# Kernel optimization log

Hardware: AMD Instinct MI355X
Metric: run time of the kernel (lower is better)

## Reference

```python
import jax, jax.numpy as jnp
import numpy as np

B, N, E, F, H, OUT = 128, 2048, 16384, 32, 64, 16


def setup_inputs() -> dict:
    key = jax.random.key(0)
    ks = jax.random.split(key, 8)
    node_features = jax.random.normal(ks[0], (B, N, F), jnp.float32)
    edge_index = jax.random.randint(ks[1], (B, 2, E), 0, N)
    n_nodes = jax.random.randint(ks[2], (B,), N // 2, N + 1)
    # prefix node mask (required for the original's index-consistency)
    node_mask = jnp.arange(N)[None, :] < n_nodes[:, None]
    glorot = lambda k, sh, fan: jax.random.normal(k, sh, jnp.float32) / np.sqrt(fan)
    return dict(
        node_features=node_features, edge_index=edge_index, node_mask=node_mask,
        W1=glorot(ks[3], (F, H), F), b1=jnp.zeros((H,), jnp.float32),
        W2=glorot(ks[4], (H, H), H), b2=jnp.zeros((H,), jnp.float32),
        aW1=glorot(ks[5], (H, H), H), ab1=jnp.zeros((H,), jnp.float32),
        aW2=glorot(ks[6], (H, OUT), H), ab2=jnp.zeros((OUT,), jnp.float32),
    )


def reference(node_features, edge_index, node_mask, W1, b1, W2, b2, aW1, ab1, aW2, ab2):
    x = node_features
    src, dst = edge_index[:, 0], edge_index[:, 1]          # [B,E] source->target
    n = node_mask.sum(-1)                                   # [B] valid nodes per graph
    max_idx = n - 1
    emask = (src <= max_idx[:, None]) & (dst <= max_idx[:, None])
    w = emask.astype(x.dtype)                               # [B,E] edge weights

    # flatten batch into one big segment space [B*N]
    offs = (jnp.arange(B, dtype=src.dtype) * N)[:, None]
    src_f = (src + offs).reshape(-1)
    dst_f = (dst + offs).reshape(-1)
    w_f = w.reshape(-1)

    # GCN normalization with self-loops (PyG GCNConv default)
    deg = jax.ops.segment_sum(w_f, dst_f, num_segments=B * N).reshape(B, N)
    deg = deg + node_mask.astype(x.dtype)                   # self-loop weight 1 on valid nodes
    dis = jnp.where(deg > 0, jax.lax.rsqrt(deg), 0.0)       # deg^{-1/2}, [B,N]
    dis_f = dis.reshape(-1)
    norm = dis_f[src_f] * dis_f[dst_f] * w_f                # [B*E]
    nmask_f = node_mask.reshape(-1).astype(x.dtype)[:, None]
    nmask = node_mask.astype(x.dtype)[..., None]

    def gcn_relu(h, W, bias):
        hW = (h @ W).reshape(B * N, -1)                     # transform first (PyG order)
        msgs = hW[src_f] * norm[:, None]                    # [B*E, H]
        agg = jax.ops.segment_sum(msgs, dst_f, num_segments=B * N)
        agg = agg + hW * ((dis * dis).reshape(-1)[:, None] * nmask_f)  # self-loop term
        out = (agg.reshape(B, N, -1) + bias) * nmask
        return jax.nn.relu(out)

    h1 = gcn_relu(x * nmask, W1, b1)
    h2 = gcn_relu(h1, W2, b2)

    # mean pool over valid nodes (zeros if empty graph)
    pooled = h2.sum(1) / jnp.maximum(n, 1)[:, None].astype(x.dtype)
    hidden = jax.nn.relu(pooled @ aW1 + ab1)
    logits = hidden @ aW2 + ab2                             # [B, OUT]
    return logits
```

## Files before the change

kernel.cpp:

```cpp
#include <hip/hip_runtime.h>
#include <hip/hip_bf16.h>

#define B 128
#define N 2048
#define E 16384
#define F 32
#define H 64
#define OUTD 16
#define CAP 16
#define NP1 (N + 1)

typedef __attribute__((ext_vector_type(8))) short bf16x8;
typedef __attribute__((ext_vector_type(4))) float f32x4;

__device__ __forceinline__ float b2f(unsigned short u) {
    return __uint_as_float(((unsigned int)u) << 16);
}
__device__ __forceinline__ unsigned short f2b(float f) {
    unsigned int x = __float_as_uint(f);
    unsigned int r = (x + 0x7FFFu + ((x >> 16) & 1u)) >> 16;
    return (unsigned short)r;
}
__device__ __forceinline__ unsigned int pack2(float a, float b) {
    return (unsigned int)f2b(a) | ((unsigned int)f2b(b) << 16);
}

__device__ __forceinline__ void unpack8(float (&a)[8], uint4 u) {
    a[0] += __uint_as_float(u.x << 16);
    a[1] += __uint_as_float(u.x & 0xffff0000u);
    a[2] += __uint_as_float(u.y << 16);
    a[3] += __uint_as_float(u.y & 0xffff0000u);
    a[4] += __uint_as_float(u.z << 16);
    a[5] += __uint_as_float(u.z & 0xffff0000u);
    a[6] += __uint_as_float(u.w << 16);
    a[7] += __uint_as_float(u.w & 0xffff0000u);
}

struct PrepArgs {
    const void* src[9];
    void* dst[9];
};

__global__ __launch_bounds__(256) void k_prep(PrepArgs pa, int* flags) {
    const int bid = blockIdx.x;
    const int t = threadIdx.x;
    int sz;
    switch (bid) {
        case 0: sz = B * N * F; break;
        case 1: sz = F * H; break;
        case 2: sz = H; break;
        case 3: sz = H * H; break;
        case 4: sz = H; break;
        case 5: sz = H * H; break;
        case 6: sz = H; break;
        case 7: sz = H * OUTD; break;
        default: sz = OUTD; break;
    }
    const int K = sz < 1024 ? sz : 1024;
    const unsigned short* p = (const unsigned short*)pa.src[bid];
    float s = 0.f;
    for (int i = t; i < K; i += 256) s += fminf(fabsf(b2f(p[i])), 1e6f);
    __shared__ float red[256];
    __shared__ int isbf;
    red[t] = s;
    __syncthreads();
    for (int st = 128; st > 0; st >>= 1) {
        if (t < st) red[t] += red[t + st];
        __syncthreads();
    }
    if (t == 0) {
        int f = (red[0] < 100.0f * (float)K) ? 1 : 0;
        isbf = f;
        if (bid == 0) flags[0] = f;
    }
    __syncthreads();
    if (bid == 0) return;
    const int fl = isbf;
    auto rd = [&](int i) -> float {
        return fl ? b2f(((const unsigned short*)pa.src[bid])[i])
                  : ((const float*)pa.src[bid])[i];
    };
    if (bid == 1) {
        unsigned short* dst = (unsigned short*)pa.dst[bid];
        for (int i = t; i < F * H; i += 256) {
            int k = i >> 6, n2 = i & 63;
            dst[n2 * 40 + k] = f2b(rd(i));
        }
    } else if (bid == 3) {
        unsigned short* dst = (unsigned short*)pa.dst[bid];
        for (int i = t; i < H * H; i += 256) {
            int k = i >> 6, n2 = i & 63;
            dst[n2 * 72 + k] = f2b(rd(i));
        }
    } else {
        float* dst = (float*)pa.dst[bid];
        for (int i = t; i < sz; i += 256) dst[i] = rd(i);
    }
}

__global__ __launch_bounds__(1024) void k_build(
    const int* __restrict__ eidx, const void* __restrict__ mask,
    int* __restrict__ n_arr, float* __restrict__ dis,
    unsigned char* __restrict__ degc, unsigned short* __restrict__ ssrc,
    int2* __restrict__ ovf, int* __restrict__ ovf_cnt,
    float* __restrict__ pooled, unsigned int* __restrict__ y_u,
    unsigned int* __restrict__ z_u) {
    __shared__ int s_cnt[N];
    __shared__ int s_w[16];
    __shared__ int s_n;
    __shared__ int s_ovf;
    const int b = blockIdx.x;
    const int t = threadIdx.x;
    const int bN = b * N;
    const unsigned char* mb = (const unsigned char*)mask;
    int mode;
    if (mb[0] == 0x80 && mb[1] == 0x3F) mode = 2;
    else if (mb[0] != 0 && mb[1] != 0) mode = 0;
    else if (mb[0] != 0) mode = (mb[4] != 0) ? 1 : 4;
    else mode = 3;
    int cnt = 0;
    if (mode == 0) {
        const unsigned char* r = mb + (size_t)b * N;
        for (int i = t; i < N; i += 1024) cnt += (r[i] != 0);
    } else if (mode == 1 || mode == 3) {
        const unsigned int* r = (const unsigned int*)mask + (size_t)b * N;
        for (int i = t; i < N; i += 1024) cnt += (r[i] != 0);
    } else if (mode == 2) {
        const unsigned short* r = (const unsigned short*)mask + (size_t)b * N;
        for (int i = t; i < N; i += 1024) cnt += (r[i] != 0);
    } else {
        const unsigned long long* r = (const unsigned long long*)mask + (size_t)b * N;
        for (int i = t; i < N; i += 1024) cnt += (r[i] != 0ULL);
    }
    for (int o = 32; o > 0; o >>= 1) cnt += __shfl_down(cnt, o);
    if ((t & 63) == 0) s_w[t >> 6] = cnt;
    for (int i = t; i < N; i += 1024) s_cnt[i] = 0;
    if (t == 0) s_ovf = 0;
    __syncthreads();
    if (t == 0) {
        int a = 0;
        for (int i = 0; i < 16; i++) a += s_w[i];
        s_n = a > N ? N : a;
    }
    __syncthreads();
    const int n = s_n;
    const int4* es4 = (const int4*)(eidx + (size_t)b * 2 * E);
    const int4* ed4 = es4 + E / 4;
    for (int i = t; i < E / 4; i += 1024) {
        int4 s4 = es4[i], d4 = ed4[i];
        if ((unsigned)s4.x < (unsigned)n && (unsigned)d4.x < (unsigned)n) atomicAdd(&s_cnt[d4.x], 1);
        if ((unsigned)s4.y < (unsigned)n && (unsigned)d4.y < (unsigned)n) atomicAdd(&s_cnt[d4.y], 1);
        if ((unsigned)s4.z < (unsigned)n && (unsigned)d4.z < (unsigned)n) atomicAdd(&s_cnt[d4.z], 1);
        if ((unsigned)s4.w < (unsigned)n && (unsigned)d4.w < (unsigned)n) atomicAdd(&s_cnt[d4.w], 1);
    }
    {
        const int4 iv = make_int4(0x08000800, 0x08000800, 0x08000800, 0x08000800);
        int4* sp4 = (int4*)(ssrc + (size_t)bN * CAP);
        for (int i = t; i < N * CAP / 8; i += 1024) sp4[i] = iv;
    }
    if (t < 16) y_u[((size_t)b * NP1 + N) * (F / 2) + t] = 0u;
    if (t >= 32 && t < 64) z_u[((size_t)b * NP1 + N) * (H / 2) + (t - 32)] = 0u;
    __syncthreads();
    for (int v = t; v < N; v += 1024) {
        int c = s_cnt[v];
        dis[bN + v] = (v < n) ? rsqrtf((float)(c + 1)) : 0.0f;
        degc[bN + v] = (unsigned char)(c < CAP ? c : CAP);
        s_cnt[v] = 0;
    }
    __syncthreads();
    for (int i = t; i < E / 4; i += 1024) {
        int4 s4 = es4[i], d4 = ed4[i];
#define FILL1(SS, DD)                                                          \
        if ((unsigned)(SS) < (unsigned)n && (unsigned)(DD) < (unsigned)n) {    \
            int pos = atomicAdd(&s_cnt[DD], 1);                                \
            if (pos < CAP)                                                     \
                ssrc[((size_t)(bN + (DD))) * CAP + pos] = (unsigned short)(SS);\
            else {                                                             \
                int oi = atomicAdd(&s_ovf, 1);                                 \
                if (oi < E) ovf[(size_t)b * E + oi] = make_int2((DD), (SS));   \
            }                                                                  \
        }
        FILL1(s4.x, d4.x) FILL1(s4.y, d4.y) FILL1(s4.z, d4.z) FILL1(s4.w, d4.w)
#undef FILL1
    }
    if (t == 0) { n_arr[b] = n; ovf_cnt[b] = s_ovf; }
    if (t < H) pooled[b * H + t] = 0.0f;
}

__global__ __launch_bounds__(256) void k_premult(
    const void* __restrict__ x, const int* __restrict__ bf16flag,
    const float* __restrict__ dis, unsigned int* __restrict__ y_u) {
    const int gid = blockIdx.x * 256 + threadIdx.x;
    const int g = gid >> 4;
    const int f2 = gid & 15;
    const int b = g >> 11;
    const int v = g & (N - 1);
    const float dv = dis[g];
    float a, c;
    if (*bf16flag) {
        const unsigned short* xp = (const unsigned short*)x + (size_t)g * F + 2 * f2;
        a = b2f(xp[0]); c = b2f(xp[1]);
    } else {
        const float* xp = (const float*)x + (size_t)g * F + 2 * f2;
        a = xp[0]; c = xp[1];
    }
    y_u[((size_t)b * NP1 + v) * (F / 2) + f2] = pack2(a * dv, c * dv);
}

__global__ __launch_bounds__(256) void k_agg_gemm1(
    const unsigned int* __restrict__ y_u, const float* __restrict__ dis,
    const unsigned char* __restrict__ degc, const unsigned short* __restrict__ ssrc,
    const int2* __restrict__ ovf, const int* __restrict__ ovf_cnt,
    const unsigned short* __restrict__ w1t, const float* __restrict__ b1f,
    unsigned short* __restrict__ zs) {
    __shared__ unsigned short s_e[64 * CAP];
    __shared__ unsigned char s_dg[64];
    __shared__ float s_dv[64];
    __shared__ float s_b1[64];
    __shared__ __align__(16) unsigned short s_w1t[64 * 40];
    __shared__ __align__(16) unsigned short s_a1[64 * 40];
    const int bid = blockIdx.x;
    const int b = (bid & 7) + ((bid >> 8) << 3);
    const int v0 = ((bid >> 3) & 31) * 64;
    const int t = threadIdx.x;
    const int bN = b * N;
    if (t < 128) ((int4*)s_e)[t] = ((const int4*)(ssrc + (size_t)(bN + v0) * CAP))[t];
    if (t >= 128 && t < 144)
        ((unsigned int*)s_dg)[t - 128] = ((const unsigned int*)(degc + bN + v0))[t - 128];
    if (t >= 192) s_dv[t - 192] = dis[bN + v0 + (t - 192)];
    if (t >= 144 && t < 208) s_b1[t - 144] = b1f[t - 144];
    for (int i = t; i < 320; i += 256) ((int4*)s_w1t)[i] = ((const int4*)w1t)[i];
    __syncthreads();
    const int lane = t & 63;
    const int w = t >> 6;
    const int oc = ovf_cnt[b];
    const unsigned int* yb = y_u + (size_t)b * NP1 * (F / 2);
    {
        const int nn = w * 16 + (lane >> 2);
        const int v = v0 + nn;
        const int cu = (lane & 3) * 4;
        int md = s_dg[w * 16 + (lane & 15)];
        int m2;
        m2 = __shfl_xor(md, 1); md = md > m2 ? md : m2;
        m2 = __shfl_xor(md, 2); md = md > m2 ? md : m2;
        m2 = __shfl_xor(md, 4); md = md > m2 ? md : m2;
        m2 = __shfl_xor(md, 8); md = md > m2 ? md : m2;
        const unsigned short* ep = &s_e[nn * CAP];
        float a[8] = {0.f, 0.f, 0.f, 0.f, 0.f, 0.f, 0.f, 0.f};
        uint4 cur = *(const uint4*)(yb + (size_t)v * (F / 2) + cu);
        uint4 nxt = *(const uint4*)(yb + (size_t)ep[0] * (F / 2) + cu);
        for (int s = 0; s < md; s++) {
            int sn = s + 1; sn = sn > CAP - 1 ? CAP - 1 : sn;
            uint4 n2 = *(const uint4*)(yb + (size_t)ep[sn] * (F / 2) + cu);
            unpack8(a, cur);
            cur = nxt; nxt = n2;
        }
        unpack8(a, cur);
        if (oc > 0) {
            const int2* ob = ovf + (size_t)b * E;
            for (int j = 0; j < oc; j++) {
                int2 o = ob[j];
                if (o.x == v) {
                    uint4 u4 = *(const uint4*)(yb + (size_t)o.y * (F / 2) + cu);
                    unpack8(a, u4);
                }
            }
        }
        const float dv = s_dv[nn];
        uint4 ov;
        ov.x = pack2(a[0] * dv, a[1] * dv);
        ov.y = pack2(a[2] * dv, a[3] * dv);
        ov.z = pack2(a[4] * dv, a[5] * dv);
        ov.w = pack2(a[6] * dv, a[7] * dv);
        *(uint4*)((unsigned int*)s_a1 + nn * 20 + cu) = ov;
    }
    __syncthreads();
    const int quad = lane >> 4;
    const int f2 = lane & 15;
    const int m0 = w * 16;
    bf16x8 af = *(const bf16x8*)&s_a1[(m0 + f2) * 40 + quad * 8];
    float dvr[4];
#pragma unroll
    for (int r = 0; r < 4; r++) dvr[r] = s_dv[m0 + quad * 4 + r];
#pragma unroll
    for (int nt = 0; nt < 4; nt++) {
        bf16x8 bf = *(const bf16x8*)&s_w1t[(nt * 16 + f2) * 40 + quad * 8];
        f32x4 acc = {0.f, 0.f, 0.f, 0.f};
        acc = __builtin_amdgcn_mfma_f32_16x16x32_bf16(af, bf, acc, 0, 0, 0);
        float bb = s_b1[nt * 16 + f2];
#pragma unroll
        for (int r = 0; r < 4; r++) {
            int row = m0 + quad * 4 + r;
            float val = dvr[r] * fmaxf(acc[r] + bb, 0.0f);
            zs[((size_t)b * NP1 + v0 + row) * H + nt * 16 + f2] = f2b(val);
        }
    }
}

__global__ __launch_bounds__(256) void k_agg_gemm2_pool(
    const unsigned int* __restrict__ z_u, const float* __restrict__ dis,
    const unsigned char* __restrict__ degc, const unsigned short* __restrict__ ssrc,
    const int2* __restrict__ ovf, const int* __restrict__ ovf_cnt,
    const unsigned short* __restrict__ w2t, const float* __restrict__ b2f_,
    float* __restrict__ pooled) {
    __shared__ unsigned short s_e[64 * CAP];
    __shared__ unsigned char s_dg[64];
    __shared__ float s_dv[64];
    __shared__ float s_b2[64];
    __shared__ __align__(16) unsigned short s_w2t[64 * 72];
    __shared__ __align__(16) unsigned short s_a2[64 * 72];
    __shared__ float s_pool[4][64];
    const int bid = blockIdx.x;
    const int b = (bid & 7) + ((bid >> 8) << 3);
    const int v0 = ((bid >> 3) & 31) * 64;
    const int t = threadIdx.x;
    const int bN = b * N;
    if (t < 128) ((int4*)s_e)[t] = ((const int4*)(ssrc + (size_t)(bN + v0) * CAP))[t];
    if (t >= 128 && t < 144)
        ((unsigned int*)s_dg)[t - 128] = ((const unsigned int*)(degc + bN + v0))[t - 128];
    if (t >= 192) s_dv[t - 192] = dis[bN + v0 + (t - 192)];
    if (t >= 144 && t < 208) s_b2[t - 144] = b2f_[t - 144];
    for (int i = t; i < 576; i += 256) ((int4*)s_w2t)[i] = ((const int4*)w2t)[i];
    __syncthreads();
    const int lane = t & 63;
    const int w = t >> 6;
    const int oc = ovf_cnt[b];
    const unsigned int* zb = z_u + (size_t)b * NP1 * (H / 2);
#pragma unroll
    for (int g = 0; g < 2; g++) {
        const int nn = w * 16 + g * 8 + (lane >> 3);
        const int v = v0 + nn;
        const int cu = (lane & 7) * 4;
        int md = s_dg[w * 16 + g * 8 + (lane & 7)];
        int m2;
        m2 = __shfl_xor(md, 1); md = md > m2 ? md : m2;
        m2 = __shfl_xor(md, 2); md = md > m2 ? md : m2;
        m2 = __shfl_xor(md, 4); md = md > m2 ? md : m2;
        const unsigned short* ep = &s_e[nn * CAP];
        float a[8] = {0.f, 0.f, 0.f, 0.f, 0.f, 0.f, 0.f, 0.f};
        uint4 cur = *(const uint4*)(zb + (size_t)v * (H / 2) + cu);
        uint4 nxt = *(const uint4*)(zb + (size_t)ep[0] * (H / 2) + cu);
        for (int s = 0; s < md; s++) {
            int sn = s + 1; sn = sn > CAP - 1 ? CAP - 1 : sn;
            uint4 n2 = *(const uint4*)(zb + (size_t)ep[sn] * (H / 2) + cu);
            unpack8(a, cur);
            cur = nxt; nxt = n2;
        }
        unpack8(a, cur);
        if (oc > 0) {
            const int2* ob = ovf + (size_t)b * E;
            for (int j = 0; j < oc; j++) {
                int2 o = ob[j];
                if (o.x == v) {
                    uint4 u4 = *(const uint4*)(zb + (size_t)o.y * (H / 2) + cu);
                    unpack8(a, u4);
                }
            }
        }
        const float dv = s_dv[nn];
        uint4 ov;
        ov.x = pack2(a[0] * dv, a[1] * dv);
        ov.y = pack2(a[2] * dv, a[3] * dv);
        ov.z = pack2(a[4] * dv, a[5] * dv);
        ov.w = pack2(a[6] * dv, a[7] * dv);
        *(uint4*)((unsigned int*)s_a2 + nn * 36 + cu) = ov;
    }
    __syncthreads();
    const int quad = lane >> 4;
    const int f2 = lane & 15;
    const int m0 = w * 16;
    bf16x8 af0 = *(const bf16x8*)&s_a2[(m0 + f2) * 72 + quad * 8];
    bf16x8 af1 = *(const bf16x8*)&s_a2[(m0 + f2) * 72 + 32 + quad * 8];
    float dvr[4];
#pragma unroll
    for (int r = 0; r < 4; r++) dvr[r] = s_dv[m0 + quad * 4 + r];
#pragma unroll
    for (int nt = 0; nt < 4; nt++) {
        bf16x8 bf0 = *(const bf16x8*)&s_w2t[(nt * 16 + f2) * 72 + quad * 8];
        bf16x8 bf1 = *(const bf16x8*)&s_w2t[(nt * 16 + f2) * 72 + 32 + quad * 8];
        f32x4 acc = {0.f, 0.f, 0.f, 0.f};
        acc = __builtin_amdgcn_mfma_f32_16x16x32_bf16(af0, bf0, acc, 0, 0, 0);
        acc = __builtin_amdgcn_mfma_f32_16x16x32_bf16(af1, bf1, acc, 0, 0, 0);
        float bb = s_b2[nt * 16 + f2];
        float ps = 0.f;
#pragma unroll
        for (int r = 0; r < 4; r++)
            ps += (dvr[r] > 0.0f) ? fmaxf(acc[r] + bb, 0.0f) : 0.0f;
        ps += __shfl_xor(ps, 16);
        ps += __shfl_xor(ps, 32);
        if (quad == 0) s_pool[w][nt * 16 + f2] = ps;
    }
    __syncthreads();
    if (t < H)
        atomicAdd(&pooled[b * H + t],
                  s_pool[0][t] + s_pool[1][t] + s_pool[2][t] + s_pool[3][t]);
}

__global__ __launch_bounds__(64) void k_mlp(
    const float* __restrict__ pooled, const int* __restrict__ n_arr,
    const float* __restrict__ aW1, const float* __restrict__ ab1,
    const float* __restrict__ aW2, const float* __restrict__ ab2,
    const int* __restrict__ flags, void* __restrict__ out) {
    const int b = blockIdx.x;
    const int t = threadIdx.x;
    __shared__ float p[64];
    __shared__ float hid[64];
    int n = n_arr[b];
    if (n < 1) n = 1;
    p[t] = pooled[b * H + t] / (float)n;
    __syncthreads();
    float acc = ab1[t];
    for (int j = 0; j < 64; j++) acc += p[j] * aW1[j * 64 + t];
    hid[t] = fmaxf(acc, 0.0f);
    __syncthreads();
    if (t < 16) {
        float a2 = ab2[t];
        for (int j = 0; j < 64; j++) a2 += hid[j] * aW2[j * 16 + t];
        if (flags[0]) ((unsigned short*)out)[b * OUTD + t] = f2b(a2);
        else          ((float*)out)[b * OUTD + t] = a2;
    }
}

extern "C" void kernel_launch(void* const* d_in, const int* in_sizes, int n_in,
                              void* d_out, int out_size, void* d_ws, size_t ws_size,
                              hipStream_t stream) {
    const void* x    = d_in[0];
    const int*  eidx = (const int*)d_in[1];
    const void* mask = d_in[2];

    char* ws = (char*)d_ws;
    size_t off = 0;
    auto alloc = [&](size_t bytes) -> void* {
        void* p = ws + off;
        off += (bytes + 255) & ~(size_t)255;
        return p;
    };
    int*   flags   = (int*)alloc(16 * sizeof(int));
    unsigned short* w1t = (unsigned short*)alloc(64 * 40 * 2);
    unsigned short* w2t = (unsigned short*)alloc(64 * 72 * 2);
    float* b1f     = (float*)alloc(H * sizeof(float));
    float* b2f_    = (float*)alloc(H * sizeof(float));
    float* aW1f    = (float*)alloc(H * H * sizeof(float));
    float* ab1f    = (float*)alloc(H * sizeof(float));
    float* aW2f    = (float*)alloc(H * OUTD * sizeof(float));
    float* ab2f    = (float*)alloc(OUTD * sizeof(float));
    int*   n_arr   = (int*)alloc(B * sizeof(int));
    float* dis     = (float*)alloc((size_t)B * N * sizeof(float));
    unsigned char*  degc = (unsigned char*)alloc((size_t)B * N);
    unsigned short* ssrc = (unsigned short*)alloc((size_t)B * N * CAP * 2);
    int2*  ovf     = (int2*)alloc((size_t)B * E * sizeof(int2));
    int*   ovf_cnt = (int*)alloc(B * sizeof(int));
    float* pooled  = (float*)alloc((size_t)B * H * sizeof(float));
    unsigned int* y_u = (unsigned int*)alloc((size_t)B * NP1 * (F / 2) * 4);
    unsigned int* z_u = (unsigned int*)alloc((size_t)B * NP1 * (H / 2) * 4);

    PrepArgs pa;
    pa.src[0] = x;        pa.dst[0] = pooled;
    pa.src[1] = d_in[3];  pa.dst[1] = w1t;
    pa.src[2] = d_in[4];  pa.dst[2] = b1f;
    pa.src[3] = d_in[5];  pa.dst[3] = w2t;
    pa.src[4] = d_in[6];  pa.dst[4] = b2f_;
    pa.src[5] = d_in[7];  pa.dst[5] = aW1f;
    pa.src[6] = d_in[8];  pa.dst[6] = ab1f;
    pa.src[7] = d_in[9];  pa.dst[7] = aW2f;
    pa.src[8] = d_in[10]; pa.dst[8] = ab2f;

    k_prep<<<9, 256, 0, stream>>>(pa, flags);
    k_build<<<B, 1024, 0, stream>>>(eidx, mask, n_arr, dis, degc, ssrc, ovf,
                                    ovf_cnt, pooled, y_u, z_u);
    k_premult<<<(B * N * (F / 2)) / 256, 256, 0, stream>>>(x, flags, dis, y_u);
    k_agg_gemm1<<<B * 32, 256, 0, stream>>>(y_u, dis, degc, ssrc, ovf, ovf_cnt,
                                            w1t, b1f, (unsigned short*)z_u);
    k_agg_gemm2_pool<<<B * 32, 256, 0, stream>>>(z_u, dis, degc, ssrc, ovf,
                                                 ovf_cnt, w2t, b2f_, pooled);
    k_mlp<<<B, 64, 0, stream>>>(pooled, n_arr, aW1f, ab1f, aW2f, ab2f, flags, d_out);
}
```

Baseline: 173.9 us.

## Fuse prep, premult and MLP into neighbouring kernels; single-pass CSR build

The weight-prep and dtype-detection kernel is merged into k_build. The separate degree-count pass over edges is dropped: slots are filled in one atomic pass and degrees are read from the final counters. The premultiply kernel is removed, so gemm1 gathers raw features and scales each neighbour by its own dis value. The MLP head runs in the last block of each graph, found with a done counter and threadfence, and the sentinel padding rows and their initialisation are removed by masking indices. This cuts three launches and one full pass over node features, in exchange for extra per-edge dis loads and a serialized tail block per graph.

```diff
diff --git a/kernel.cpp b/kernel.cpp
--- a/kernel.cpp
+++ b/kernel.cpp
@@ -8,7 +8,6 @@
 #define H 64
 #define OUTD 16
 #define CAP 16
-#define NP1 (N + 1)
 
 typedef __attribute__((ext_vector_type(8))) short bf16x8;
 typedef __attribute__((ext_vector_type(4))) float f32x4;
@@ -25,7 +24,17 @@
     return (unsigned int)f2b(a) | ((unsigned int)f2b(b) << 16);
 }
 
-__device__ __forceinline__ void unpack8(float (&a)[8], uint4 u) {
+__device__ __forceinline__ void fma8(float (&a)[8], uint4 u, float w) {
+    a[0] = fmaf(__uint_as_float(u.x << 16), w, a[0]);
+    a[1] = fmaf(__uint_as_float(u.x & 0xffff0000u), w, a[1]);
+    a[2] = fmaf(__uint_as_float(u.y << 16), w, a[2]);
+    a[3] = fmaf(__uint_as_float(u.y & 0xffff0000u), w, a[3]);
+    a[4] = fmaf(__uint_as_float(u.z << 16), w, a[4]);
+    a[5] = fmaf(__uint_as_float(u.z & 0xffff0000u), w, a[5]);
+    a[6] = fmaf(__uint_as_float(u.w << 16), w, a[6]);
+    a[7] = fmaf(__uint_as_float(u.w & 0xffff0000u), w, a[7]);
+}
+__device__ __forceinline__ void add8(float (&a)[8], uint4 u) {
     a[0] += __uint_as_float(u.x << 16);
     a[1] += __uint_as_float(u.x & 0xffff0000u);
     a[2] += __uint_as_float(u.y << 16);
@@ -41,77 +50,35 @@
     void* dst[9];
 };
 
-__global__ __launch_bounds__(256) void k_prep(PrepArgs pa, int* flags) {
-    const int bid = blockIdx.x;
-    const int t = threadIdx.x;
-    int sz;
-    switch (bid) {
-        case 0: sz = B * N * F; break;
-        case 1: sz = F * H; break;
-        case 2: sz = H; break;
-        case 3: sz = H * H; break;
-        case 4: sz = H; break;
-        case 5: sz = H * H; break;
-        case 6: sz = H; break;
-        case 7: sz = H * OUTD; break;
-        default: sz = OUTD; break;
-    }
-    const int K = sz < 1024 ? sz : 1024;
-    const unsigned short* p = (const unsigned short*)pa.src[bid];
-    float s = 0.f;
-    for (int i = t; i < K; i += 256) s += fminf(fabsf(b2f(p[i])), 1e6f);
-    __shared__ float red[256];
-    __shared__ int isbf;
-    red[t] = s;
-    __syncthreads();
-    for (int st = 128; st > 0; st >>= 1) {
-        if (t < st) red[t] += red[t + st];
-        __syncthreads();
-    }
-    if (t == 0) {
-        int f = (red[0] < 100.0f * (float)K) ? 1 : 0;
-        isbf = f;
-        if (bid == 0) flags[0] = f;
-    }
-    __syncthreads();
-    if (bid == 0) return;
-    const int fl = isbf;
-    auto rd = [&](int i) -> float {
-        return fl ? b2f(((const unsigned short*)pa.src[bid])[i])
-                  : ((const float*)pa.src[bid])[i];
-    };
-    if (bid == 1) {
-        unsigned short* dst = (unsigned short*)pa.dst[bid];
-        for (int i = t; i < F * H; i += 256) {
-            int k = i >> 6, n2 = i & 63;
-            dst[n2 * 40 + k] = f2b(rd(i));
-        }
-    } else if (bid == 3) {
-        unsigned short* dst = (unsigned short*)pa.dst[bid];
-        for (int i = t; i < H * H; i += 256) {
-            int k = i >> 6, n2 = i & 63;
-            dst[n2 * 72 + k] = f2b(rd(i));
-        }
-    } else {
-        float* dst = (float*)pa.dst[bid];
-        for (int i = t; i < sz; i += 256) dst[i] = rd(i);
-    }
-}
-
 __global__ __launch_bounds__(1024) void k_build(
-    const int* __restrict__ eidx, const void* __restrict__ mask,
+    const void* __restrict__ x, const int* __restrict__ eidx,
+    const void* __restrict__ mask, PrepArgs pa, int* __restrict__ flags,
     int* __restrict__ n_arr, float* __restrict__ dis,
     unsigned char* __restrict__ degc, unsigned short* __restrict__ ssrc,
     int2* __restrict__ ovf, int* __restrict__ ovf_cnt,
-    float* __restrict__ pooled, unsigned int* __restrict__ y_u,
-    unsigned int* __restrict__ z_u) {
+    float* __restrict__ pooled, int* __restrict__ done,
+    unsigned int* __restrict__ y_u) {
     __shared__ int s_cnt[N];
+    __shared__ float s_fred[16];
     __shared__ int s_w[16];
-    __shared__ int s_n;
-    __shared__ int s_ovf;
+    __shared__ int s_n, s_ovf, s_xbf, s_pf;
     const int b = blockIdx.x;
     const int t = threadIdx.x;
     const int bN = b * N;
+    {
+        const unsigned short* p = (const unsigned short*)x;
+        float s = (t < 1024) ? fminf(fabsf(b2f(p[t])), 1e6f) : 0.f;
+        for (int o = 32; o > 0; o >>= 1) s += __shfl_down(s, o);
+        if ((t & 63) == 0) s_fred[t >> 6] = s;
+        __syncthreads();
+        if (t == 0) {
+            float a = 0.f;
+            for (int i = 0; i < 16; i++) a += s_fred[i];
+            int f = (a < 100.0f * 1024.0f) ? 1 : 0;
+            s_xbf = f;
+            if (b == 0) flags[0] = f;
+        }
+    }
     const unsigned char* mb = (const unsigned char*)mask;
     int mode;
     if (mb[0] == 0x80 && mb[1] == 0x3F) mode = 2;
@@ -135,39 +102,17 @@
     for (int o = 32; o > 0; o >>= 1) cnt += __shfl_down(cnt, o);
     if ((t & 63) == 0) s_w[t >> 6] = cnt;
     for (int i = t; i < N; i += 1024) s_cnt[i] = 0;
-    if (t == 0) s_ovf = 0;
     __syncthreads();
     if (t == 0) {
         int a = 0;
         for (int i = 0; i < 16; i++) a += s_w[i];
         s_n = a > N ? N : a;
+        s_ovf = 0;
     }
     __syncthreads();
     const int n = s_n;
     const int4* es4 = (const int4*)(eidx + (size_t)b * 2 * E);
     const int4* ed4 = es4 + E / 4;
-    for (int i = t; i < E / 4; i += 1024) {
-        int4 s4 = es4[i], d4 = ed4[i];
-        if ((unsigned)s4.x < (unsigned)n && (unsigned)d4.x < (unsigned)n) atomicAdd(&s_cnt[d4.x], 1);
-        if ((unsigned)s4.y < (unsigned)n && (unsigned)d4.y < (unsigned)n) atomicAdd(&s_cnt[d4.y], 1);
-        if ((unsigned)s4.z < (unsigned)n && (unsigned)d4.z < (unsigned)n) atomicAdd(&s_cnt[d4.z], 1);
-        if ((unsigned)s4.w < (unsigned)n && (unsigned)d4.w < (unsigned)n) atomicAdd(&s_cnt[d4.w], 1);
-    }
-    {
-        const int4 iv = make_int4(0x08000800, 0x08000800, 0x08000800, 0x08000800);
-        int4* sp4 = (int4*)(ssrc + (size_t)bN * CAP);
-        for (int i = t; i < N * CAP / 8; i += 1024) sp4[i] = iv;
-    }
-    if (t < 16) y_u[((size_t)b * NP1 + N) * (F / 2) + t] = 0u;
-    if (t >= 32 && t < 64) z_u[((size_t)b * NP1 + N) * (H / 2) + (t - 32)] = 0u;
-    __syncthreads();
-    for (int v = t; v < N; v += 1024) {
-        int c = s_cnt[v];
-        dis[bN + v] = (v < n) ? rsqrtf((float)(c + 1)) : 0.0f;
-        degc[bN + v] = (unsigned char)(c < CAP ? c : CAP);
-        s_cnt[v] = 0;
-    }
-    __syncthreads();
     for (int i = t; i < E / 4; i += 1024) {
         int4 s4 = es4[i], d4 = ed4[i];
 #define FILL1(SS, DD)                                                          \
@@ -183,37 +128,79 @@
         FILL1(s4.x, d4.x) FILL1(s4.y, d4.y) FILL1(s4.z, d4.z) FILL1(s4.w, d4.w)
 #undef FILL1
     }
-    if (t == 0) { n_arr[b] = n; ovf_cnt[b] = s_ovf; }
+    __syncthreads();
+    for (int v = t; v < N; v += 1024) {
+        int c = s_cnt[v];
+        dis[bN + v] = (v < n) ? rsqrtf((float)(c + 1)) : 0.0f;
+        degc[bN + v] = (unsigned char)(c < CAP ? c : CAP);
+    }
     if (t < H) pooled[b * H + t] = 0.0f;
-}
-
-__global__ __launch_bounds__(256) void k_premult(
-    const void* __restrict__ x, const int* __restrict__ bf16flag,
-    const float* __restrict__ dis, unsigned int* __restrict__ y_u) {
-    const int gid = blockIdx.x * 256 + threadIdx.x;
-    const int g = gid >> 4;
-    const int f2 = gid & 15;
-    const int b = g >> 11;
-    const int v = g & (N - 1);
-    const float dv = dis[g];
-    float a, c;
-    if (*bf16flag) {
-        const unsigned short* xp = (const unsigned short*)x + (size_t)g * F + 2 * f2;
-        a = b2f(xp[0]); c = b2f(xp[1]);
-    } else {
-        const float* xp = (const float*)x + (size_t)g * F + 2 * f2;
-        a = xp[0]; c = xp[1];
-    }
-    y_u[((size_t)b * NP1 + v) * (F / 2) + f2] = pack2(a * dv, c * dv);
+    if (t == 0) { n_arr[b] = n; ovf_cnt[b] = s_ovf; done[b] = 0; }
+    if (!s_xbf) {
+        const float4* xp = (const float4*)((const float*)x + (size_t)bN * F);
+        uint2* yp = (uint2*)(y_u + (size_t)bN * (F / 2));
+        for (int i = t; i < N * F / 4; i += 1024) {
+            float4 v = xp[i];
+            yp[i] = make_uint2(pack2(v.x, v.y), pack2(v.z, v.w));
+        }
+    }
+    if (b >= 1 && b <= 8) {
+        int sz;
+        switch (b) {
+            case 1: sz = F * H; break;
+            case 2: sz = H; break;
+            case 3: sz = H * H; break;
+            case 4: sz = H; break;
+            case 5: sz = H * H; break;
+            case 6: sz = H; break;
+            case 7: sz = H * OUTD; break;
+            default: sz = OUTD; break;
+        }
+        const int K = sz < 1024 ? sz : 1024;
+        const unsigned short* p = (const unsigned short*)pa.src[b];
+        float s = (t < K) ? fminf(fabsf(b2f(p[t])), 1e6f) : 0.f;
+        for (int o = 32; o > 0; o >>= 1) s += __shfl_down(s, o);
+        __syncthreads();
+        if ((t & 63) == 0) s_fred[t >> 6] = s;
+        __syncthreads();
+        if (t == 0) {
+            float a = 0.f;
+            for (int i = 0; i < 16; i++) a += s_fred[i];
+            s_pf = (a < 100.0f * (float)K) ? 1 : 0;
+        }
+        __syncthreads();
+        const int fl = s_pf;
+        auto rd = [&](int i) -> float {
+            return fl ? b2f(((const unsigned short*)pa.src[b])[i])
+                      : ((const float*)pa.src[b])[i];
+        };
+        if (b == 1) {
+            unsigned short* dst = (unsigned short*)pa.dst[b];
+            for (int i = t; i < F * H; i += 1024) {
+                int k = i >> 6, n2 = i & 63;
+                dst[n2 * 40 + k] = f2b(rd(i));
+            }
+        } else if (b == 3) {
+            unsigned short* dst = (unsigned short*)pa.dst[b];
+            for (int i = t; i < H * H; i += 1024) {
+                int k = i >> 6, n2 = i & 63;
+                dst[n2 * 72 + k] = f2b(rd(i));
+            }
+        } else {
+            float* dst = (float*)pa.dst[b];
+            for (int i = t; i < sz; i += 1024) dst[i] = rd(i);
+        }
+    }
 }
 
 __global__ __launch_bounds__(256) void k_agg_gemm1(
-    const unsigned int* __restrict__ y_u, const float* __restrict__ dis,
+    const void* __restrict__ x, const unsigned int* __restrict__ y_conv,
+    const int* __restrict__ flags, const float* __restrict__ dis,
     const unsigned char* __restrict__ degc, const unsigned short* __restrict__ ssrc,
     const int2* __restrict__ ovf, const int* __restrict__ ovf_cnt,
     const unsigned short* __restrict__ w1t, const float* __restrict__ b1f,
     unsigned short* __restrict__ zs) {
-    __shared__ unsigned short s_e[64 * CAP];
+    __shared__ unsigned short s_e[64 * CAP + 32];
     __shared__ unsigned char s_dg[64];
     __shared__ float s_dv[64];
     __shared__ float s_b1[64];
@@ -234,45 +221,45 @@
     const int lane = t & 63;
     const int w = t >> 6;
     const int oc = ovf_cnt[b];
-    const unsigned int* yb = y_u + (size_t)b * NP1 * (F / 2);
+    const unsigned int* yb =
+        (flags[0] ? (const unsigned int*)x : y_conv) + (size_t)bN * (F / 2);
+    const float* disb = dis + bN;
     {
         const int nn = w * 16 + (lane >> 2);
         const int v = v0 + nn;
         const int cu = (lane & 3) * 4;
-        int md = s_dg[w * 16 + (lane & 15)];
-        int m2;
-        m2 = __shfl_xor(md, 1); md = md > m2 ? md : m2;
-        m2 = __shfl_xor(md, 2); md = md > m2 ? md : m2;
-        m2 = __shfl_xor(md, 4); md = md > m2 ? md : m2;
-        m2 = __shfl_xor(md, 8); md = md > m2 ? md : m2;
+        const int dg = s_dg[nn];
+        const float dv = s_dv[nn];
         const unsigned short* ep = &s_e[nn * CAP];
         float a[8] = {0.f, 0.f, 0.f, 0.f, 0.f, 0.f, 0.f, 0.f};
-        uint4 cur = *(const uint4*)(yb + (size_t)v * (F / 2) + cu);
-        uint4 nxt = *(const uint4*)(yb + (size_t)ep[0] * (F / 2) + cu);
-        for (int s = 0; s < md; s++) {
-            int sn = s + 1; sn = sn > CAP - 1 ? CAP - 1 : sn;
-            uint4 n2 = *(const uint4*)(yb + (size_t)ep[sn] * (F / 2) + cu);
-            unpack8(a, cur);
-            cur = nxt; nxt = n2;
-        }
-        unpack8(a, cur);
+        uint4 rs = *(const uint4*)(yb + (size_t)v * (F / 2) + cu);
+        fma8(a, rs, dv);
+        for (int s = 0; s < dg; s += 2) {
+            int i0 = ep[s] & (N - 1);
+            int i1 = ep[s + 1] & (N - 1);
+            float w0 = disb[i0];
+            float w1 = (s + 1 < dg) ? disb[i1] : 0.f;
+            uint4 r0 = *(const uint4*)(yb + (size_t)i0 * (F / 2) + cu);
+            uint4 r1 = *(const uint4*)(yb + (size_t)i1 * (F / 2) + cu);
+            fma8(a, r0, w0);
+            fma8(a, r1, w1);
+        }
         if (oc > 0) {
             const int2* ob = ovf + (size_t)b * E;
             for (int j = 0; j < oc; j++) {
                 int2 o = ob[j];
                 if (o.x == v) {
                     uint4 u4 = *(const uint4*)(yb + (size_t)o.y * (F / 2) + cu);
-                    unpack8(a, u4);
+                    fma8(a, u4, disb[o.y]);
                 }
             }
         }
-        const float dv = s_dv[nn];
-        uint4 ov;
-        ov.x = pack2(a[0] * dv, a[1] * dv);
-        ov.y = pack2(a[2] * dv, a[3] * dv);
-        ov.z = pack2(a[4] * dv, a[5] * dv);
-        ov.w = pack2(a[6] * dv, a[7] * dv);
-        *(uint4*)((unsigned int*)s_a1 + nn * 20 + cu) = ov;
+        uint4 ovv;
+        ovv.x = pack2(a[0] * dv, a[1] * dv);
+        ovv.y = pack2(a[2] * dv, a[3] * dv);
+        ovv.z = pack2(a[4] * dv, a[5] * dv);
+        ovv.w = pack2(a[6] * dv, a[7] * dv);
+        *(uint4*)((unsigned int*)s_a1 + nn * 20 + cu) = ovv;
     }
     __syncthreads();
     const int quad = lane >> 4;
@@ -292,7 +279,7 @@
         for (int r = 0; r < 4; r++) {
             int row = m0 + quad * 4 + r;
             float val = dvr[r] * fmaxf(acc[r] + bb, 0.0f);
-            zs[((size_t)b * NP1 + v0 + row) * H + nt * 16 + f2] = f2b(val);
+            zs[(size_t)(bN + v0 + row) * H + nt * 16 + f2] = f2b(val);
         }
     }
 }
@@ -302,14 +289,20 @@
     const unsigned char* __restrict__ degc, const unsigned short* __restrict__ ssrc,
     const int2* __restrict__ ovf, const int* __restrict__ ovf_cnt,
     const unsigned short* __restrict__ w2t, const float* __restrict__ b2f_,
-    float* __restrict__ pooled) {
-    __shared__ unsigned short s_e[64 * CAP];
+    float* __restrict__ pooled, int* __restrict__ done,
+    const int* __restrict__ n_arr, const float* __restrict__ aW1,
+    const float* __restrict__ ab1, const float* __restrict__ aW2,
+    const float* __restrict__ ab2, const int* __restrict__ flags,
+    void* __restrict__ out) {
+    __shared__ unsigned short s_e[64 * CAP + 32];
     __shared__ unsigned char s_dg[64];
     __shared__ float s_dv[64];
     __shared__ float s_b2[64];
     __shared__ __align__(16) unsigned short s_w2t[64 * 72];
     __shared__ __align__(16) unsigned short s_a2[64 * 72];
     __shared__ float s_pool[4][64];
+    __shared__ float s_p[64], s_h[64];
+    __shared__ int s_last;
     const int bid = blockIdx.x;
     const int b = (bid & 7) + ((bid >> 8) << 3);
     const int v0 = ((bid >> 3) & 31) * 64;
@@ -325,45 +318,43 @@
     const int lane = t & 63;
     const int w = t >> 6;
     const int oc = ovf_cnt[b];
-    const unsigned int* zb = z_u + (size_t)b * NP1 * (H / 2);
+    const unsigned int* zb = z_u + (size_t)bN * (H / 2);
 #pragma unroll
     for (int g = 0; g < 2; g++) {
         const int nn = w * 16 + g * 8 + (lane >> 3);
         const int v = v0 + nn;
         const int cu = (lane & 7) * 4;
-        int md = s_dg[w * 16 + g * 8 + (lane & 7)];
-        int m2;
-        m2 = __shfl_xor(md, 1); md = md > m2 ? md : m2;
-        m2 = __shfl_xor(md, 2); md = md > m2 ? md : m2;
-        m2 = __shfl_xor(md, 4); md = md > m2 ? md : m2;
+        const int dg = s_dg[nn];
         const unsigned short* ep = &s_e[nn * CAP];
         float a[8] = {0.f, 0.f, 0.f, 0.f, 0.f, 0.f, 0.f, 0.f};
-        uint4 cur = *(const uint4*)(zb + (size_t)v * (H / 2) + cu);
-        uint4 nxt = *(const uint4*)(zb + (size_t)ep[0] * (H / 2) + cu);
-        for (int s = 0; s < md; s++) {
-            int sn = s + 1; sn = sn > CAP - 1 ? CAP - 1 : sn;
-            uint4 n2 = *(const uint4*)(zb + (size_t)ep[sn] * (H / 2) + cu);
-            unpack8(a, cur);
-            cur = nxt; nxt = n2;
-        }
-        unpack8(a, cur);
+        uint4 rs = *(const uint4*)(zb + (size_t)v * (H / 2) + cu);
+        add8(a, rs);
+        for (int s = 0; s < dg; s += 2) {
+            int i0 = ep[s] & (N - 1);
+            int i1 = ep[s + 1] & (N - 1);
+            float w1 = (s + 1 < dg) ? 1.0f : 0.f;
+            uint4 r0 = *(const uint4*)(zb + (size_t)i0 * (H / 2) + cu);
+            uint4 r1 = *(const uint4*)(zb + (size_t)i1 * (H / 2) + cu);
+            add8(a, r0);
+            fma8(a, r1, w1);
+        }
         if (oc > 0) {
             const int2* ob = ovf + (size_t)b * E;
             for (int j = 0; j < oc; j++) {
                 int2 o = ob[j];
                 if (o.x == v) {
                     uint4 u4 = *(const uint4*)(zb + (size_t)o.y * (H / 2) + cu);
-                    unpack8(a, u4);
+                    add8(a, u4);
                 }
             }
         }
         const float dv = s_dv[nn];
-        uint4 ov;
-        ov.x = pack2(a[0] * dv, a[1] * dv);
-        ov.y = pack2(a[2] * dv, a[3] * dv);
-        ov.z = pack2(a[4] * dv, a[5] * dv);
-        ov.w = pack2(a[6] * dv, a[7] * dv);
-        *(uint4*)((unsigned int*)s_a2 + nn * 36 + cu) = ov;
+        uint4 ovv;
+        ovv.x = pack2(a[0] * dv, a[1] * dv);
+        ovv.y = pack2(a[2] * dv, a[3] * dv);
+        ovv.z = pack2(a[4] * dv, a[5] * dv);
+        ovv.w = pack2(a[6] * dv, a[7] * dv);
+        *(uint4*)((unsigned int*)s_a2 + nn * 36 + cu) = ovv;
     }
     __syncthreads();
     const int quad = lane >> 4;
@@ -394,30 +385,24 @@
     if (t < H)
         atomicAdd(&pooled[b * H + t],
                   s_pool[0][t] + s_pool[1][t] + s_pool[2][t] + s_pool[3][t]);
-}
-
-__global__ __launch_bounds__(64) void k_mlp(
-    const float* __restrict__ pooled, const int* __restrict__ n_arr,
-    const float* __restrict__ aW1, const float* __restrict__ ab1,
-    const float* __restrict__ aW2, const float* __restrict__ ab2,
-    const int* __restrict__ flags, void* __restrict__ out) {
-    const int b = blockIdx.x;
-    const int t = threadIdx.x;
-    __shared__ float p[64];
-    __shared__ float hid[64];
-    int n = n_arr[b];
-    if (n < 1) n = 1;
-    p[t] = pooled[b * H + t] / (float)n;
-    __syncthreads();
-    float acc = ab1[t];
-    for (int j = 0; j < 64; j++) acc += p[j] * aW1[j * 64 + t];
-    hid[t] = fmaxf(acc, 0.0f);
-    __syncthreads();
-    if (t < 16) {
-        float a2 = ab2[t];
-        for (int j = 0; j < 64; j++) a2 += hid[j] * aW2[j * 16 + t];
-        if (flags[0]) ((unsigned short*)out)[b * OUTD + t] = f2b(a2);
-        else          ((float*)out)[b * OUTD + t] = a2;
+    __syncthreads();
+    __threadfence();
+    if (t == 0) s_last = (atomicAdd(&done[b], 1) == 31) ? 1 : 0;
+    __syncthreads();
+    if (s_last && t < 64) {
+        float pv = atomicAdd(&pooled[b * H + t], 0.0f);
+        int n = n_arr[b];
+        if (n < 1) n = 1;
+        s_p[t] = pv / (float)n;
+        float acc = ab1[t];
+        for (int j = 0; j < 64; j++) acc += s_p[j] * aW1[j * 64 + t];
+        s_h[t] = fmaxf(acc, 0.0f);
+        if (t < 16) {
+            float a2 = ab2[t];
+            for (int j = 0; j < 64; j++) a2 += s_h[j] * aW2[j * 16 + t];
+            if (flags[0]) ((unsigned short*)out)[b * OUTD + t] = f2b(a2);
+            else          ((float*)out)[b * OUTD + t] = a2;
+        }
     }
 }
 
@@ -445,14 +430,15 @@
     float* aW2f    = (float*)alloc(H * OUTD * sizeof(float));
     float* ab2f    = (float*)alloc(OUTD * sizeof(float));
     int*   n_arr   = (int*)alloc(B * sizeof(int));
+    int*   done    = (int*)alloc(B * sizeof(int));
     float* dis     = (float*)alloc((size_t)B * N * sizeof(float));
     unsigned char*  degc = (unsigned char*)alloc((size_t)B * N);
     unsigned short* ssrc = (unsigned short*)alloc((size_t)B * N * CAP * 2);
     int2*  ovf     = (int2*)alloc((size_t)B * E * sizeof(int2));
     int*   ovf_cnt = (int*)alloc(B * sizeof(int));
     float* pooled  = (float*)alloc((size_t)B * H * sizeof(float));
-    unsigned int* y_u = (unsigned int*)alloc((size_t)B * NP1 * (F / 2) * 4);
-    unsigned int* z_u = (unsigned int*)alloc((size_t)B * NP1 * (H / 2) * 4);
+    unsigned int* y_u = (unsigned int*)alloc((size_t)B * N * (F / 2) * 4);
+    unsigned int* z_u = (unsigned int*)alloc((size_t)B * N * (H / 2) * 4);
 
     PrepArgs pa;
     pa.src[0] = x;        pa.dst[0] = pooled;
@@ -465,13 +451,13 @@
     pa.src[7] = d_in[9];  pa.dst[7] = aW2f;
     pa.src[8] = d_in[10]; pa.dst[8] = ab2f;
 
-    k_prep<<<9, 256, 0, stream>>>(pa, flags);
-    k_build<<<B, 1024, 0, stream>>>(eidx, mask, n_arr, dis, degc, ssrc, ovf,
-                                    ovf_cnt, pooled, y_u, z_u);
-    k_premult<<<(B * N * (F / 2)) / 256, 256, 0, stream>>>(x, flags, dis, y_u);
-    k_agg_gemm1<<<B * 32, 256, 0, stream>>>(y_u, dis, degc, ssrc, ovf, ovf_cnt,
-                                            w1t, b1f, (unsigned short*)z_u);
+    k_build<<<B, 1024, 0, stream>>>(x, eidx, mask, pa, flags, n_arr, dis, degc,
+                                    ssrc, ovf, ovf_cnt, pooled, done, y_u);
+    k_agg_gemm1<<<B * 32, 256, 0, stream>>>(x, y_u, flags, dis, degc, ssrc, ovf,
+                                            ovf_cnt, w1t, b1f,
+                                            (unsigned short*)z_u);
     k_agg_gemm2_pool<<<B * 32, 256, 0, stream>>>(z_u, dis, degc, ssrc, ovf,
-                                                 ovf_cnt, w2t, b2f_, pooled);
-    k_mlp<<<B, 64, 0, stream>>>(pooled, n_arr, aW1f, ab1f, aW2f, ab2f, flags, d_out);
-}
+                                                 ovf_cnt, w2t, b2f_, pooled,
+                                                 done, n_arr, aW1f, ab1f, aW2f,
+                                                 ab2f, flags, d_out);
+}
```

Measured after the change: 468.6 us. 2.7x slower.
